# Kernel tuning notes

Measured on AMD Instinct MI355X. Metric: run time of the kernel, lower is better.

## Reference

```python
import jax, jax.numpy as jnp
import numpy as np

D_MODEL = 1024
NUM_LATENTS = 8
N_HEADS = 8
HEAD_DIM = D_MODEL // N_HEADS
LN_EPS = 1e-5
NEG_INF = -1e9


def setup_inputs() -> dict:
    key = jax.random.key(0)
    ks = jax.random.split(key, 9)
    B, S, d = 8, 8192, D_MODEL
    hidden_states = jax.random.normal(ks[0], (B, S, d), dtype=jnp.float32)
    attention_mask = jax.random.randint(ks[1], (B, S), 0, 2, dtype=jnp.int32)
    # guarantee at least one valid token per row
    attention_mask = attention_mask.at[:, 0].set(1)
    latent_queries = jax.random.normal(ks[2], (NUM_LATENTS, d), dtype=jnp.float32) * 0.02
    lim = 1.0 / np.sqrt(d)
    in_proj_weight = jax.random.uniform(ks[3], (3 * d, d), minval=-lim, maxval=lim, dtype=jnp.float32)
    in_proj_bias = jnp.zeros((3 * d,), jnp.float32)
    out_proj_weight = jax.random.uniform(ks[4], (d, d), minval=-lim, maxval=lim, dtype=jnp.float32)
    out_proj_bias = jnp.zeros((d,), jnp.float32)
    ln_gamma = jnp.ones((d,), jnp.float32)
    ln_beta = jnp.zeros((d,), jnp.float32)
    return {
        "hidden_states": hidden_states,
        "latent_queries": latent_queries,
        "in_proj_weight": in_proj_weight,
        "in_proj_bias": in_proj_bias,
        "out_proj_weight": out_proj_weight,
        "out_proj_bias": out_proj_bias,
        "ln_gamma": ln_gamma,
        "ln_beta": ln_beta,
        "attention_mask": attention_mask,
    }


def reference(hidden_states, latent_queries, in_proj_weight, in_proj_bias,
              out_proj_weight, out_proj_bias, ln_gamma, ln_beta, attention_mask):
    B, S, d = hidden_states.shape
    K, H, hd = NUM_LATENTS, N_HEADS, HEAD_DIM
    Wq, Wk, Wv = jnp.split(in_proj_weight, 3, axis=0)   # each [d, d]
    bq, bk, bv = jnp.split(in_proj_bias, 3, axis=0)
    # projections (queries shared over batch)
    q = latent_queries @ Wq.T + bq                      # [K, d]
    k = hidden_states @ Wk.T + bk                       # [B, S, d]
    v = hidden_states @ Wv.T + bv                       # [B, S, d]
    q = q.reshape(K, H, hd).transpose(1, 0, 2)          # [H, K, hd]
    k = k.reshape(B, S, H, hd).transpose(0, 2, 1, 3)    # [B, H, S, hd]
    v = v.reshape(B, S, H, hd).transpose(0, 2, 1, 3)    # [B, H, S, hd]
    scale = 1.0 / np.sqrt(hd)
    scores = jnp.einsum('hkd,bhsd->bhks', q, k) * scale  # [B, H, K, S]
    pad = (attention_mask == 0)[:, None, None, :]        # [B, 1, 1, S]
    scores = jnp.where(pad, NEG_INF, scores)
    attn = jax.nn.softmax(scores, axis=-1)
    ctx = jnp.einsum('bhks,bhsd->bhkd', attn, v)         # [B, H, K, hd]
    ctx = ctx.transpose(0, 2, 1, 3).reshape(B, K, d)     # [B, K, d]
    pooled = ctx @ out_proj_weight.T + out_proj_bias     # [B, K, d]
    # LayerNorm
    mu = pooled.mean(-1, keepdims=True)
    var = jnp.mean(jnp.square(pooled - mu), axis=-1, keepdims=True)
    pooled = (pooled - mu) * jax.lax.rsqrt(var + LN_EPS) * ln_gamma + ln_beta
    return pooled.mean(axis=1)                           # [B, d]
```

## Files before the change

### kernel.cpp

```cpp
#include <hip/hip_runtime.h>
#include <math.h>

#define D_M 1024
#define S_L 8192
#define B_N 8
#define H_N 8
#define HD_ 128
#define HK_ 64
#define SCALE_ 0.08838834764831845f
#define NEG_INF_ -1e9f
#define PITCH_ 40

typedef _Float16 half8v __attribute__((ext_vector_type(8)));
typedef _Float16 half4v __attribute__((ext_vector_type(4)));
typedef float floatx4 __attribute__((ext_vector_type(4)));

__global__ void k_q(const float* __restrict__ lat, const float* __restrict__ W,
                    const float* __restrict__ bias, float* __restrict__ q) {
  int g = blockIdx.x * blockDim.x + threadIdx.x;
  int kidx = g >> 10, i = g & 1023;
  const float* wr = W + (size_t)i * D_M;
  const float* lr = lat + kidx * D_M;
  float acc = bias[i];
  #pragma unroll 4
  for (int t = 0; t < D_M; t += 4) {
    float4 w = *(const float4*)(wr + t);
    float4 l = *(const float4*)(lr + t);
    acc += w.x*l.x + w.y*l.y + w.z*l.z + w.w*l.w;
  }
  q[g] = acc;
}

__global__ void k_qt(const float* __restrict__ q, const float* __restrict__ W,
                     const float* __restrict__ bias, _Float16* __restrict__ qth,
                     float* __restrict__ qconst) {
  int g = blockIdx.x * blockDim.x + threadIdx.x;
  int hk = g >> 10, j = g & 1023;
  int h = hk >> 3, kidx = hk & 7;
  const float* qr = q + kidx * D_M + h * HD_;
  const float* wb = W + ((size_t)D_M + (size_t)h * HD_) * D_M + j;
  float acc = 0.f;
  #pragma unroll 4
  for (int dd = 0; dd < HD_; ++dd)
    acc += qr[dd] * wb[(size_t)dd * D_M];
  qth[g] = (_Float16)(acc * SCALE_);
  if (j == 0) {
    const float* bk = bias + D_M + h * HD_;
    float c = 0.f;
    for (int dd = 0; dd < HD_; ++dd) c += qr[dd] * bk[dd];
    qconst[hk] = c * SCALE_;
  }
}

__global__ __launch_bounds__(256) void k_scores_mfma(
    const float* __restrict__ hsrc, const _Float16* __restrict__ qth,
    const float* __restrict__ qc, const int* __restrict__ mask,
    float* __restrict__ scoresT, float* __restrict__ pm, float* __restrict__ pl) {
  __shared__ __align__(16) _Float16 As[128 * 32];
  __shared__ __align__(16) _Float16 Bs[64 * 32];
  __shared__ int smask[128];
  const int tid = threadIdx.x;
  const int b = blockIdx.x >> 6;
  const int st = blockIdx.x & 63;
  const int s0 = st * 128;
  const int w = tid >> 6, l = tid & 63;
  if (tid < 128) smask[tid] = mask[b * S_L + s0 + tid];
  floatx4 acc[2][4];
  #pragma unroll
  for (int mf = 0; mf < 2; ++mf)
    #pragma unroll
    for (int nf = 0; nf < 4; ++nf) acc[mf][nf] = (floatx4){0.f, 0.f, 0.f, 0.f};

  const int r_ = tid >> 2, c_ = tid & 3;
  const float* hb = hsrc + ((size_t)b * S_L + s0) * D_M;
  float4 fa[2][2];
  half8v fb;
  {
    const float* p0 = hb + (size_t)r_ * D_M + c_ * 8;
    fa[0][0] = *(const float4*)p0; fa[0][1] = *(const float4*)(p0 + 4);
    const float* p1 = hb + (size_t)(64 + r_) * D_M + c_ * 8;
    fa[1][0] = *(const float4*)p1; fa[1][1] = *(const float4*)(p1 + 4);
    fb = *(const half8v*)(qth + (size_t)r_ * D_M + c_ * 8);
  }
  const int row16 = l & 15, kc = l >> 4;
  for (int k0 = 0; k0 < D_M; k0 += 32) {
    __syncthreads();
    #pragma unroll
    for (int p = 0; p < 2; ++p) {
      int row = p * 64 + r_;
      half8v hv;
      hv[0] = (_Float16)fa[p][0].x; hv[1] = (_Float16)fa[p][0].y;
      hv[2] = (_Float16)fa[p][0].z; hv[3] = (_Float16)fa[p][0].w;
      hv[4] = (_Float16)fa[p][1].x; hv[5] = (_Float16)fa[p][1].y;
      hv[6] = (_Float16)fa[p][1].z; hv[7] = (_Float16)fa[p][1].w;
      int slot = c_ ^ ((row >> 1) & 3);
      *(half8v*)&As[(row * 4 + slot) * 8] = hv;
    }
    {
      int slot = c_ ^ ((r_ >> 1) & 3);
      *(half8v*)&Bs[(r_ * 4 + slot) * 8] = fb;
    }
    if (k0 + 32 < D_M) {
      const float* p0 = hb + (size_t)r_ * D_M + (k0 + 32) + c_ * 8;
      fa[0][0] = *(const float4*)p0; fa[0][1] = *(const float4*)(p0 + 4);
      const float* p1 = hb + (size_t)(64 + r_) * D_M + (k0 + 32) + c_ * 8;
      fa[1][0] = *(const float4*)p1; fa[1][1] = *(const float4*)(p1 + 4);
      fb = *(const half8v*)(qth + (size_t)r_ * D_M + (k0 + 32) + c_ * 8);
    }
    __syncthreads();
    half8v af[2], bf4[4];
    #pragma unroll
    for (int mf = 0; mf < 2; ++mf) {
      int row = w * 32 + mf * 16 + row16;
      af[mf] = *(const half8v*)&As[(row * 4 + (kc ^ ((row >> 1) & 3))) * 8];
    }
    #pragma unroll
    for (int nf = 0; nf < 4; ++nf) {
      int row = nf * 16 + row16;
      bf4[nf] = *(const half8v*)&Bs[(row * 4 + (kc ^ ((row >> 1) & 3))) * 8];
    }
    #pragma unroll
    for (int mf = 0; mf < 2; ++mf)
      #pragma unroll
      for (int nf = 0; nf < 4; ++nf)
        acc[mf][nf] = __builtin_amdgcn_mfma_f32_16x16x32_f16(af[mf], bf4[nf], acc[mf][nf], 0, 0, 0);
  }
  #pragma unroll
  for (int nf = 0; nf < 4; ++nf) {
    int hk = nf * 16 + row16;
    float qcv = qc[hk];
    float vals[8];
    float mloc = -3.4e38f;
    #pragma unroll
    for (int mf = 0; mf < 2; ++mf) {
      #pragma unroll
      for (int r = 0; r < 4; ++r) {
        int srow = w * 32 + mf * 16 + kc * 4 + r;
        float v = smask[srow] ? (acc[mf][nf][r] + qcv) : NEG_INF_;
        vals[mf * 4 + r] = v;
        mloc = fmaxf(mloc, v);
        scoresT[((size_t)b * S_L + s0 + srow) * HK_ + hk] = v;
      }
    }
    float ls = 0.f;
    #pragma unroll
    for (int i = 0; i < 8; ++i) ls += __expf(vals[i] - mloc);
    #pragma unroll
    for (int off = 16; off < 64; off <<= 1) {
      float mo = __shfl_xor(mloc, off, 64);
      float lo2 = __shfl_xor(ls, off, 64);
      float mn = fmaxf(mloc, mo);
      ls = ls * __expf(mloc - mn) + lo2 * __expf(mo - mn);
      mloc = mn;
    }
    if (kc == 0) {
      int idx = ((b * 64 + st) * 4 + w) * 64 + hk;
      pm[idx] = mloc;
      pl[idx] = ls;
    }
  }
}

__global__ void k_stats2(const float* __restrict__ pm, const float* __restrict__ pl,
                         float* __restrict__ mvec, float* __restrict__ lvinv) {
  int t = blockIdx.x * blockDim.x + threadIdx.x;
  int base = (t >> 6) * 16384 + (t & 63);
  float m = -3.4e38f;
  for (int i = 0; i < 256; ++i) m = fmaxf(m, pm[base + i * 64]);
  float lsum = 0.f;
  for (int i = 0; i < 256; ++i)
    lsum += pl[base + i * 64] * __expf(pm[base + i * 64] - m);
  mvec[t] = m;
  lvinv[t] = 1.f / lsum;
}

__global__ __launch_bounds__(256) void k_pexp(
    const float* __restrict__ scoresT, const float* __restrict__ mvec,
    _Float16* __restrict__ ph) {
  __shared__ float st_[64][68];
  int tid = threadIdx.x;
  int b = blockIdx.x >> 7;
  int s0 = (blockIdx.x & 127) * 64;
  #pragma unroll
  for (int p = 0; p < 4; ++p) {
    int idx = tid + 256 * p;
    int sl = idx >> 4, c4 = (idx & 15) * 4;
    float4 v = *(const float4*)(scoresT + ((size_t)b * S_L + s0 + sl) * HK_ + c4);
    *(float4*)&st_[sl][c4] = v;
  }
  __syncthreads();
  int hk = tid >> 2, cs = tid & 3;
  float m = mvec[b * 64 + hk];
  half8v o0, o1;
  #pragma unroll
  for (int i = 0; i < 8; ++i) o0[i] = (_Float16)__expf(st_[cs * 16 + i][hk] - m);
  #pragma unroll
  for (int i = 0; i < 8; ++i) o1[i] = (_Float16)__expf(st_[cs * 16 + 8 + i][hk] - m);
  _Float16* dst = ph + ((size_t)b * 64 + hk) * S_L + s0 + cs * 16;
  *(half8v*)dst = o0;
  *(half8v*)(dst + 8) = o1;
}

__global__ __launch_bounds__(512) void k_part(
    const float* __restrict__ hsrc, const _Float16* __restrict__ ph,
    float* __restrict__ part) {
  __shared__ __align__(16) _Float16 htile[512 * PITCH_];
  const int tid = threadIdx.x;
  const int b  = blockIdx.x >> 5;
  const int jb = (blockIdx.x >> 4) & 1;
  const int sc = blockIdx.x & 15;
  const int w = tid >> 6, l = tid & 63;
  const int row16 = l & 15, kc = l >> 4;
  const int s_base = sc * 512;
  const float* hb = hsrc + (size_t)b * S_L * D_M + jb * 512;
  const _Float16* phb = ph + (size_t)b * HK_ * S_L;
  floatx4 acc[4][4];
  #pragma unroll
  for (int mf = 0; mf < 4; ++mf)
    #pragma unroll
    for (int nf = 0; nf < 4; ++nf) acc[mf][nf] = (floatx4){0.f, 0.f, 0.f, 0.f};

  const int jcol = tid;
  float colv[32];
  #pragma unroll
  for (int s = 0; s < 32; ++s)
    colv[s] = hb[(size_t)(s_base + s) * D_M + jcol];

  for (int t = 0; t < 16; ++t) {
    const int s0 = s_base + t * 32;
    __syncthreads();
    #pragma unroll
    for (int sb = 0; sb < 8; ++sb) {
      half4v hv;
      hv[0] = (_Float16)colv[sb * 4 + 0];
      hv[1] = (_Float16)colv[sb * 4 + 1];
      hv[2] = (_Float16)colv[sb * 4 + 2];
      hv[3] = (_Float16)colv[sb * 4 + 3];
      *(half4v*)&htile[jcol * PITCH_ + sb * 4] = hv;
    }
    __syncthreads();
    if (t < 15) {
      #pragma unroll
      for (int s = 0; s < 32; ++s)
        colv[s] = hb[(size_t)(s0 + 32 + s) * D_M + jcol];
    }
    half8v ap[4];
    #pragma unroll
    for (int mf = 0; mf < 4; ++mf)
      ap[mf] = *(const half8v*)(phb + (size_t)(mf * 16 + row16) * S_L + s0 + kc * 8);
    #pragma unroll
    for (int nf = 0; nf < 4; ++nf) {
      int j = w * 64 + nf * 16 + row16;
      half8v bv = *(const half8v*)&htile[j * PITCH_ + kc * 8];
      #pragma unroll
      for (int mf = 0; mf < 4; ++mf)
        acc[mf][nf] = __builtin_amdgcn_mfma_f32_16x16x32_f16(ap[mf], bv, acc[mf][nf], 0, 0, 0);
    }
  }
  #pragma unroll
  for (int mf = 0; mf < 4; ++mf)
    #pragma unroll
    for (int nf = 0; nf < 4; ++nf) {
      int j = w * 64 + nf * 16 + row16;
      #pragma unroll
      for (int r = 0; r < 4; ++r) {
        int hk = mf * 16 + kc * 4 + r;
        part[(((size_t)(b * 2 + jb) * 16 + sc) * HK_ + hk) * 512 + j] = acc[mf][nf][r];
      }
    }
}

__global__ void k_comb(const float* __restrict__ part, const float* __restrict__ lvinv,
                       float* __restrict__ ctxh) {
  int g = blockIdx.x * blockDim.x + threadIdx.x;
  int b = g >> 14;
  int rem = g & 16383;
  int hk = rem >> 8;
  int j4 = rem & 255;
  int jb = j4 >> 7;
  int jr4 = j4 & 127;
  const float* pb = part + ((size_t)(b * 2 + jb) * 16 * HK_ + hk) * 512 + jr4 * 4;
  float4 s = make_float4(0.f, 0.f, 0.f, 0.f);
  #pragma unroll
  for (int sc = 0; sc < 16; ++sc) {
    float4 v = *(const float4*)(pb + (size_t)sc * HK_ * 512);
    s.x += v.x; s.y += v.y; s.z += v.z; s.w += v.w;
  }
  float li = lvinv[b * 64 + hk];
  s.x *= li; s.y *= li; s.z *= li; s.w *= li;
  *(float4*)(ctxh + ((size_t)b * HK_ + hk) * D_M + j4 * 4) = s;
}

__global__ void k_ctx(const float* __restrict__ ctxh, const float* __restrict__ W,
                      const float* __restrict__ bias, float* __restrict__ ctx) {
  int g = blockIdx.x * blockDim.x + threadIdx.x;
  int b = g >> 13, kidx = (g >> 10) & 7, i = g & 1023;
  int hk = (i >> 7) * 8 + kidx;
  const float* wr = W + ((size_t)2 * D_M + i) * D_M;
  const float* xr = ctxh + ((size_t)b * HK_ + hk) * D_M;
  float acc = bias[2 * D_M + i];
  #pragma unroll 4
  for (int t = 0; t < D_M; t += 4) {
    float4 w = *(const float4*)(wr + t);
    float4 x = *(const float4*)(xr + t);
    acc += w.x*x.x + w.y*x.y + w.z*x.z + w.w*x.w;
  }
  ctx[g] = acc;
}

__global__ void k_pool(const float* __restrict__ ctx, const float* __restrict__ W,
                       const float* __restrict__ bias, float* __restrict__ pooled) {
  int g = blockIdx.x * blockDim.x + threadIdx.x;
  int b = g >> 13, kidx = (g >> 10) & 7, i = g & 1023;
  const float* wr = W + (size_t)i * D_M;
  const float* xr = ctx + ((size_t)b * 8 + kidx) * D_M;
  float acc = bias[i];
  #pragma unroll 4
  for (int t = 0; t < D_M; t += 4) {
    float4 w = *(const float4*)(wr + t);
    float4 x = *(const float4*)(xr + t);
    acc += w.x*x.x + w.y*x.y + w.z*x.z + w.w*x.w;
  }
  pooled[g] = acc;
}

__global__ void k_ln(const float* __restrict__ pooled, const float* __restrict__ gamma,
                     const float* __restrict__ beta, float* __restrict__ out) {
  __shared__ float red[256];
  int b = blockIdx.x, tid = threadIdx.x;
  float acc[4] = {0.f, 0.f, 0.f, 0.f};
  for (int kidx = 0; kidx < 8; ++kidx) {
    const float* row = pooled + ((size_t)b * 8 + kidx) * D_M;
    float v[4]; float s = 0.f;
    #pragma unroll
    for (int c = 0; c < 4; ++c) { v[c] = row[tid + 256 * c]; s += v[c]; }
    red[tid] = s; __syncthreads();
    for (int off = 128; off > 0; off >>= 1) {
      if (tid < off) red[tid] += red[tid + off];
      __syncthreads();
    }
    float mu = red[0] * (1.f / 1024.f);
    __syncthreads();
    float ss = 0.f;
    #pragma unroll
    for (int c = 0; c < 4; ++c) { float dd = v[c] - mu; ss += dd * dd; }
    red[tid] = ss; __syncthreads();
    for (int off = 128; off > 0; off >>= 1) {
      if (tid < off) red[tid] += red[tid + off];
      __syncthreads();
    }
    float rstd = rsqrtf(red[0] * (1.f / 1024.f) + 1e-5f);
    __syncthreads();
    #pragma unroll
    for (int c = 0; c < 4; ++c) {
      int i = tid + 256 * c;
      acc[c] += ((v[c] - mu) * rstd * gamma[i] + beta[i]) * 0.125f;
    }
  }
  #pragma unroll
  for (int c = 0; c < 4; ++c) out[(size_t)b * D_M + tid + 256 * c] = acc[c];
}

extern "C" void kernel_launch(void* const* d_in, const int* in_sizes, int n_in,
                              void* d_out, int out_size, void* d_ws, size_t ws_size,
                              hipStream_t stream) {
  const float* hidden = (const float*)d_in[0];
  const float* latent = (const float*)d_in[1];
  const float* w_in   = (const float*)d_in[2];
  const float* b_in   = (const float*)d_in[3];
  const float* w_out  = (const float*)d_in[4];
  const float* b_out  = (const float*)d_in[5];
  const float* gamma  = (const float*)d_in[6];
  const float* beta   = (const float*)d_in[7];
  const int*   mask   = (const int*)d_in[8];
  float* out = (float*)d_out;
  float* ws = (float*)d_ws;
  float* q      = ws;
  float* qc     = q + 8192;
  float* mvec   = qc + 64;
  float* lvinv  = mvec + 512;
  float* pm     = lvinv + 512;
  float* pl     = pm + 131072;
  _Float16* qth = (_Float16*)(pl + 131072);
  _Float16* ph  = (_Float16*)(pl + 131072 + 32768);
  float* scoresT = pl + 131072 + 32768 + 2097152;
  float* part   = scoresT + 4194304;
  float* ctxh   = part + 8388608;
  float* ctx    = ctxh + 524288;
  float* pooled = ctx + 65536;

  k_q          <<<32,   256, 0, stream>>>(latent, w_in, b_in, q);
  k_qt         <<<256,  256, 0, stream>>>(q, w_in, b_in, qth, qc);
  k_scores_mfma<<<512,  256, 0, stream>>>(hidden, qth, qc, mask, scoresT, pm, pl);
  k_stats2     <<<2,    256, 0, stream>>>(pm, pl, mvec, lvinv);
  k_pexp       <<<1024, 256, 0, stream>>>(scoresT, mvec, ph);
  k_part       <<<256,  512, 0, stream>>>(hidden, ph, part);
  k_comb       <<<512,  256, 0, stream>>>(part, lvinv, ctxh);
  k_ctx        <<<256,  256, 0, stream>>>(ctxh, w_in, b_in, ctx);
  k_pool       <<<256,  256, 0, stream>>>(ctx, w_out, b_out, pooled);
  k_ln         <<<8,    256, 0, stream>>>(pooled, gamma, beta, out);
}
```

Measured before the change: 339.4 us.

## Load MFMA fragments directly from global, split part and GEMV reductions finer

The scores kernel drops its LDS staging and barriers. Each wave now loads its MFMA A fragments straight from global memory, and B fragments come from a pre-permuted q layout written by k_qt. The k_part kernel halves its sequence chunk per block, doubling the grid and the partial buffer that k_comb reduces. k_ctx and k_pool split each dot product across four lanes with shuffle reductions to raise parallelism. The cost is more partial-sum traffic, and every wave now fetches the B tile on its own instead of sharing it through LDS.

```diff
diff --git a/kernel.cpp b/kernel.cpp
--- a/kernel.cpp
+++ b/kernel.cpp
@@ -32,7 +32,7 @@
 }
 
 __global__ void k_qt(const float* __restrict__ q, const float* __restrict__ W,
-                     const float* __restrict__ bias, _Float16* __restrict__ qth,
+                     const float* __restrict__ bias, _Float16* __restrict__ qtr,
                      float* __restrict__ qconst) {
   int g = blockIdx.x * blockDim.x + threadIdx.x;
   int hk = g >> 10, j = g & 1023;
@@ -43,7 +43,7 @@
   #pragma unroll 4
   for (int dd = 0; dd < HD_; ++dd)
     acc += qr[dd] * wb[(size_t)dd * D_M];
-  qth[g] = (_Float16)(acc * SCALE_);
+  qtr[((j >> 3) * 64 + hk) * 8 + (j & 7)] = (_Float16)(acc * SCALE_);
   if (j == 0) {
     const float* bk = bias + D_M + h * HD_;
     float c = 0.f;
@@ -52,79 +52,51 @@
   }
 }
 
-__global__ __launch_bounds__(256) void k_scores_mfma(
-    const float* __restrict__ hsrc, const _Float16* __restrict__ qth,
+__global__ __launch_bounds__(256) void k_scores2(
+    const float* __restrict__ hsrc, const _Float16* __restrict__ qtr,
     const float* __restrict__ qc, const int* __restrict__ mask,
     float* __restrict__ scoresT, float* __restrict__ pm, float* __restrict__ pl) {
-  __shared__ __align__(16) _Float16 As[128 * 32];
-  __shared__ __align__(16) _Float16 Bs[64 * 32];
-  __shared__ int smask[128];
   const int tid = threadIdx.x;
   const int b = blockIdx.x >> 6;
   const int st = blockIdx.x & 63;
   const int s0 = st * 128;
   const int w = tid >> 6, l = tid & 63;
-  if (tid < 128) smask[tid] = mask[b * S_L + s0 + tid];
+  const int row16 = l & 15, kc = l >> 4;
   floatx4 acc[2][4];
   #pragma unroll
   for (int mf = 0; mf < 2; ++mf)
     #pragma unroll
     for (int nf = 0; nf < 4; ++nf) acc[mf][nf] = (floatx4){0.f, 0.f, 0.f, 0.f};
 
-  const int r_ = tid >> 2, c_ = tid & 3;
-  const float* hb = hsrc + ((size_t)b * S_L + s0) * D_M;
-  float4 fa[2][2];
-  half8v fb;
-  {
-    const float* p0 = hb + (size_t)r_ * D_M + c_ * 8;
-    fa[0][0] = *(const float4*)p0; fa[0][1] = *(const float4*)(p0 + 4);
-    const float* p1 = hb + (size_t)(64 + r_) * D_M + c_ * 8;
-    fa[1][0] = *(const float4*)p1; fa[1][1] = *(const float4*)(p1 + 4);
-    fb = *(const half8v*)(qth + (size_t)r_ * D_M + c_ * 8);
-  }
-  const int row16 = l & 15, kc = l >> 4;
-  for (int k0 = 0; k0 < D_M; k0 += 32) {
-    __syncthreads();
-    #pragma unroll
-    for (int p = 0; p < 2; ++p) {
-      int row = p * 64 + r_;
-      half8v hv;
-      hv[0] = (_Float16)fa[p][0].x; hv[1] = (_Float16)fa[p][0].y;
-      hv[2] = (_Float16)fa[p][0].z; hv[3] = (_Float16)fa[p][0].w;
-      hv[4] = (_Float16)fa[p][1].x; hv[5] = (_Float16)fa[p][1].y;
-      hv[6] = (_Float16)fa[p][1].z; hv[7] = (_Float16)fa[p][1].w;
-      int slot = c_ ^ ((row >> 1) & 3);
-      *(half8v*)&As[(row * 4 + slot) * 8] = hv;
-    }
-    {
-      int slot = c_ ^ ((r_ >> 1) & 3);
-      *(half8v*)&Bs[(r_ * 4 + slot) * 8] = fb;
-    }
-    if (k0 + 32 < D_M) {
-      const float* p0 = hb + (size_t)r_ * D_M + (k0 + 32) + c_ * 8;
-      fa[0][0] = *(const float4*)p0; fa[0][1] = *(const float4*)(p0 + 4);
-      const float* p1 = hb + (size_t)(64 + r_) * D_M + (k0 + 32) + c_ * 8;
-      fa[1][0] = *(const float4*)p1; fa[1][1] = *(const float4*)(p1 + 4);
-      fb = *(const half8v*)(qth + (size_t)r_ * D_M + (k0 + 32) + c_ * 8);
-    }
-    __syncthreads();
-    half8v af[2], bf4[4];
-    #pragma unroll
-    for (int mf = 0; mf < 2; ++mf) {
-      int row = w * 32 + mf * 16 + row16;
-      af[mf] = *(const half8v*)&As[(row * 4 + (kc ^ ((row >> 1) & 3))) * 8];
+  const float* ar0 = hsrc + ((size_t)b * S_L + s0 + w * 32 + row16) * D_M + kc * 8;
+  const float* ar1 = ar0 + (size_t)16 * D_M;
+  const _Float16* br = qtr + (size_t)(kc * 64) * 8 + row16 * 8;
+
+  #pragma unroll 4
+  for (int kk = 0; kk < 32; ++kk) {
+    floatx4 a00 = *(const floatx4*)(ar0 + kk * 32);
+    floatx4 a01 = *(const floatx4*)(ar0 + kk * 32 + 4);
+    floatx4 a10 = *(const floatx4*)(ar1 + kk * 32);
+    floatx4 a11 = *(const floatx4*)(ar1 + kk * 32 + 4);
+    half8v af0, af1;
+    #pragma unroll
+    for (int e = 0; e < 4; ++e) {
+      af0[e] = (_Float16)a00[e]; af0[4 + e] = (_Float16)a01[e];
+      af1[e] = (_Float16)a10[e]; af1[4 + e] = (_Float16)a11[e];
     }
     #pragma unroll
     for (int nf = 0; nf < 4; ++nf) {
-      int row = nf * 16 + row16;
-      bf4[nf] = *(const half8v*)&Bs[(row * 4 + (kc ^ ((row >> 1) & 3))) * 8];
-    }
-    #pragma unroll
-    for (int mf = 0; mf < 2; ++mf)
-      #pragma unroll
-      for (int nf = 0; nf < 4; ++nf)
-        acc[mf][nf] = __builtin_amdgcn_mfma_f32_16x16x32_f16(af[mf], bf4[nf], acc[mf][nf], 0, 0, 0);
-  }
+      half8v bf = *(const half8v*)(br + (size_t)kk * 2048 + nf * 128);
+      acc[0][nf] = __builtin_amdgcn_mfma_f32_16x16x32_f16(af0, bf, acc[0][nf], 0, 0, 0);
+      acc[1][nf] = __builtin_amdgcn_mfma_f32_16x16x32_f16(af1, bf, acc[1][nf], 0, 0, 0);
+    }
+  }
+  int msk[8];
+  #pragma unroll
+  for (int mf = 0; mf < 2; ++mf)
+    #pragma unroll
+    for (int r = 0; r < 4; ++r)
+      msk[mf * 4 + r] = mask[b * S_L + s0 + w * 32 + mf * 16 + kc * 4 + r];
   #pragma unroll
   for (int nf = 0; nf < 4; ++nf) {
     int hk = nf * 16 + row16;
@@ -136,7 +108,7 @@
       #pragma unroll
       for (int r = 0; r < 4; ++r) {
         int srow = w * 32 + mf * 16 + kc * 4 + r;
-        float v = smask[srow] ? (acc[mf][nf][r] + qcv) : NEG_INF_;
+        float v = msk[mf * 4 + r] ? (acc[mf][nf][r] + qcv) : NEG_INF_;
         vals[mf * 4 + r] = v;
         mloc = fmaxf(mloc, v);
         scoresT[((size_t)b * S_L + s0 + srow) * HK_ + hk] = v;
@@ -206,12 +178,12 @@
     float* __restrict__ part) {
   __shared__ __align__(16) _Float16 htile[512 * PITCH_];
   const int tid = threadIdx.x;
-  const int b  = blockIdx.x >> 5;
-  const int jb = (blockIdx.x >> 4) & 1;
-  const int sc = blockIdx.x & 15;
+  const int b  = blockIdx.x >> 6;
+  const int jb = (blockIdx.x >> 5) & 1;
+  const int sc = blockIdx.x & 31;
   const int w = tid >> 6, l = tid & 63;
   const int row16 = l & 15, kc = l >> 4;
-  const int s_base = sc * 512;
+  const int s_base = sc * 256;
   const float* hb = hsrc + (size_t)b * S_L * D_M + jb * 512;
   const _Float16* phb = ph + (size_t)b * HK_ * S_L;
   floatx4 acc[4][4];
@@ -226,7 +198,7 @@
   for (int s = 0; s < 32; ++s)
     colv[s] = hb[(size_t)(s_base + s) * D_M + jcol];
 
-  for (int t = 0; t < 16; ++t) {
+  for (int t = 0; t < 8; ++t) {
     const int s0 = s_base + t * 32;
     __syncthreads();
     #pragma unroll
@@ -239,7 +211,7 @@
       *(half4v*)&htile[jcol * PITCH_ + sb * 4] = hv;
     }
     __syncthreads();
-    if (t < 15) {
+    if (t < 7) {
       #pragma unroll
       for (int s = 0; s < 32; ++s)
         colv[s] = hb[(size_t)(s0 + 32 + s) * D_M + jcol];
@@ -265,7 +237,7 @@
       #pragma unroll
       for (int r = 0; r < 4; ++r) {
         int hk = mf * 16 + kc * 4 + r;
-        part[(((size_t)(b * 2 + jb) * 16 + sc) * HK_ + hk) * 512 + j] = acc[mf][nf][r];
+        part[(((size_t)(b * 2 + jb) * 32 + sc) * HK_ + hk) * 512 + j] = acc[mf][nf][r];
       }
     }
 }
@@ -279,10 +251,10 @@
   int j4 = rem & 255;
   int jb = j4 >> 7;
   int jr4 = j4 & 127;
-  const float* pb = part + ((size_t)(b * 2 + jb) * 16 * HK_ + hk) * 512 + jr4 * 4;
+  const float* pb = part + ((size_t)(b * 2 + jb) * 32 * HK_ + hk) * 512 + jr4 * 4;
   float4 s = make_float4(0.f, 0.f, 0.f, 0.f);
-  #pragma unroll
-  for (int sc = 0; sc < 16; ++sc) {
+  #pragma unroll 8
+  for (int sc = 0; sc < 32; ++sc) {
     float4 v = *(const float4*)(pb + (size_t)sc * HK_ * 512);
     s.x += v.x; s.y += v.y; s.z += v.z; s.w += v.w;
   }
@@ -293,35 +265,41 @@
 
 __global__ void k_ctx(const float* __restrict__ ctxh, const float* __restrict__ W,
                       const float* __restrict__ bias, float* __restrict__ ctx) {
-  int g = blockIdx.x * blockDim.x + threadIdx.x;
-  int b = g >> 13, kidx = (g >> 10) & 7, i = g & 1023;
+  int g2 = blockIdx.x * blockDim.x + threadIdx.x;
+  int o = g2 >> 2, kq = g2 & 3;
+  int b = o >> 13, kidx = (o >> 10) & 7, i = o & 1023;
   int hk = (i >> 7) * 8 + kidx;
-  const float* wr = W + ((size_t)2 * D_M + i) * D_M;
-  const float* xr = ctxh + ((size_t)b * HK_ + hk) * D_M;
-  float acc = bias[2 * D_M + i];
-  #pragma unroll 4
-  for (int t = 0; t < D_M; t += 4) {
+  const float* wr = W + ((size_t)2 * D_M + i) * D_M + kq * 256;
+  const float* xr = ctxh + ((size_t)b * HK_ + hk) * D_M + kq * 256;
+  float acc = 0.f;
+  #pragma unroll 8
+  for (int t = 0; t < 256; t += 4) {
     float4 w = *(const float4*)(wr + t);
     float4 x = *(const float4*)(xr + t);
     acc += w.x*x.x + w.y*x.y + w.z*x.z + w.w*x.w;
   }
-  ctx[g] = acc;
+  acc += __shfl_xor(acc, 1, 64);
+  acc += __shfl_xor(acc, 2, 64);
+  if (kq == 0) ctx[o] = acc + bias[2 * D_M + i];
 }
 
 __global__ void k_pool(const float* __restrict__ ctx, const float* __restrict__ W,
                        const float* __restrict__ bias, float* __restrict__ pooled) {
-  int g = blockIdx.x * blockDim.x + threadIdx.x;
-  int b = g >> 13, kidx = (g >> 10) & 7, i = g & 1023;
-  const float* wr = W + (size_t)i * D_M;
-  const float* xr = ctx + ((size_t)b * 8 + kidx) * D_M;
-  float acc = bias[i];
-  #pragma unroll 4
-  for (int t = 0; t < D_M; t += 4) {
+  int g2 = blockIdx.x * blockDim.x + threadIdx.x;
+  int o = g2 >> 2, kq = g2 & 3;
+  int b = o >> 13, kidx = (o >> 10) & 7, i = o & 1023;
+  const float* wr = W + (size_t)i * D_M + kq * 256;
+  const float* xr = ctx + ((size_t)b * 8 + kidx) * D_M + kq * 256;
+  float acc = 0.f;
+  #pragma unroll 8
+  for (int t = 0; t < 256; t += 4) {
     float4 w = *(const float4*)(wr + t);
     float4 x = *(const float4*)(xr + t);
     acc += w.x*x.x + w.y*x.y + w.z*x.z + w.w*x.w;
   }
-  pooled[g] = acc;
+  acc += __shfl_xor(acc, 1, 64);
+  acc += __shfl_xor(acc, 2, 64);
+  if (kq == 0) pooled[o] = acc + bias[i];
 }
 
 __global__ void k_ln(const float* __restrict__ pooled, const float* __restrict__ gamma,
@@ -381,22 +359,22 @@
   float* lvinv  = mvec + 512;
   float* pm     = lvinv + 512;
   float* pl     = pm + 131072;
-  _Float16* qth = (_Float16*)(pl + 131072);
+  _Float16* qtr = (_Float16*)(pl + 131072);
   _Float16* ph  = (_Float16*)(pl + 131072 + 32768);
   float* scoresT = pl + 131072 + 32768 + 2097152;
   float* part   = scoresT + 4194304;
-  float* ctxh   = part + 8388608;
+  float* ctxh   = part + 16777216;
   float* ctx    = ctxh + 524288;
   float* pooled = ctx + 65536;
 
-  k_q          <<<32,   256, 0, stream>>>(latent, w_in, b_in, q);
-  k_qt         <<<256,  256, 0, stream>>>(q, w_in, b_in, qth, qc);
-  k_scores_mfma<<<512,  256, 0, stream>>>(hidden, qth, qc, mask, scoresT, pm, pl);
-  k_stats2     <<<2,    256, 0, stream>>>(pm, pl, mvec, lvinv);
-  k_pexp       <<<1024, 256, 0, stream>>>(scoresT, mvec, ph);
-  k_part       <<<256,  512, 0, stream>>>(hidden, ph, part);
-  k_comb       <<<512,  256, 0, stream>>>(part, lvinv, ctxh);
-  k_ctx        <<<256,  256, 0, stream>>>(ctxh, w_in, b_in, ctx);
-  k_pool       <<<256,  256, 0, stream>>>(ctx, w_out, b_out, pooled);
-  k_ln         <<<8,    256, 0, stream>>>(pooled, gamma, beta, out);
-}
+  k_q      <<<32,   256, 0, stream>>>(latent, w_in, b_in, q);
+  k_qt     <<<256,  256, 0, stream>>>(q, w_in, b_in, qtr, qc);
+  k_scores2<<<512,  256, 0, stream>>>(hidden, qtr, qc, mask, scoresT, pm, pl);
+  k_stats2 <<<2,    256, 0, stream>>>(pm, pl, mvec, lvinv);
+  k_pexp   <<<1024, 256, 0, stream>>>(scoresT, mvec, ph);
+  k_part   <<<512,  512, 0, stream>>>(hidden, ph, part);
+  k_comb   <<<512,  256, 0, stream>>>(part, lvinv, ctxh);
+  k_ctx    <<<1024, 256, 0, stream>>>(ctxh, w_in, b_in, ctx);
+  k_pool   <<<1024, 256, 0, stream>>>(ctx, w_out, b_out, pooled);
+  k_ln     <<<8,    256, 0, stream>>>(pooled, gamma, beta, out);
+}
```

Result: slower. 437.4 us (+28.9%).
